# Kernel optimization log

Hardware: AMD Instinct MI355X
Metric: run time of the kernel (lower is better)

## Reference

```python
import jax, jax.numpy as jnp
import numpy as np

NUM_EMBEDDINGS = 1024
EMBEDDING_DIM = 256
SPLIT = 8
SPLIT_DIM = EMBEDDING_DIM // SPLIT  # 32
COMMITMENT_COST = 0.25
DECAY = 0.99
EPSILON = 1e-05


def setup_inputs() -> dict:
    key = jax.random.key(0)
    k1, k2, k3 = jax.random.split(key, 3)
    inputs = jax.random.normal(k1, (16384, EMBEDDING_DIM), dtype=jnp.float32)
    embedding = jax.random.normal(k2, (NUM_EMBEDDINGS, SPLIT_DIM), dtype=jnp.float32)
    ema_cluster_size = jnp.zeros((NUM_EMBEDDINGS,), dtype=jnp.float32)
    ema_w = jax.random.normal(k3, (NUM_EMBEDDINGS, SPLIT_DIM), dtype=jnp.float32)
    return {"inputs": inputs, "embedding": embedding,
            "ema_cluster_size": ema_cluster_size, "ema_w": ema_w}


def reference(inputs, embedding, ema_cluster_size, ema_w):
    B = inputs.shape[0]
    flat = inputs.reshape(-1, SPLIT_DIM)  # [B*split, d]
    rows = flat.shape[0]

    # squared euclidean distances to codebook: [rows, K]
    distances = (jnp.sum(flat ** 2, axis=1, keepdims=True)
                 + jnp.sum(embedding ** 2, axis=1)
                 - 2.0 * flat @ embedding.T)
    idx = jnp.argmin(distances, axis=1)  # [rows]

    # one-hot @ embedding == gather (same math, efficient form)
    quantized_flat = embedding[idx]  # [rows, d]

    # EMA statistics (training-mode update); quantization uses the OLD weights,
    # exactly as in the torch forward.
    counts = jax.ops.segment_sum(jnp.ones((rows,), jnp.float32), idx,
                                 num_segments=NUM_EMBEDDINGS)
    dw = jax.ops.segment_sum(flat, idx, num_segments=NUM_EMBEDDINGS)  # enc.T @ flat
    new_cs = ema_cluster_size * DECAY + (1.0 - DECAY) * counts
    n = jnp.sum(new_cs)
    new_cs = (new_cs + EPSILON) / (n + NUM_EMBEDDINGS * EPSILON) * n
    new_ema_w = ema_w * DECAY + (1.0 - DECAY) * dw
    new_embedding = new_ema_w / new_cs[:, None]

    # losses (EMA variant: only commitment term)
    e_latent_loss = jnp.mean((jax.lax.stop_gradient(quantized_flat) - flat) ** 2)
    loss = COMMITMENT_COST * e_latent_loss

    # straight-through estimator
    quantized_flat = flat + jax.lax.stop_gradient(quantized_flat - flat)
    quantized = quantized_flat.reshape(B, -1)  # [B, EMBEDDING_DIM]

    avg_probs = counts / rows  # mean of one-hot encodings over rows
    perplexity = jnp.exp(-jnp.sum(avg_probs * jnp.log(avg_probs + 1e-10)))

    encoding_indices = idx.reshape(B, SPLIT)
    return (loss, quantized, perplexity, encoding_indices,
            new_embedding, new_cs, new_ema_w)
```

## Files before the change

kernel.cpp:

```cpp
#include <hip/hip_runtime.h>

#define NUM_CODES 1024
#define DIM 32
#define ROWS 131072
#define DECAYF 0.99f
#define EPSF 1e-5f
#define CCOST 0.25f
#define SLAB 33792
#define RGROUPS 8
#define IBLK (SLAB / 256)

typedef __attribute__((ext_vector_type(8))) short short8v;
typedef __attribute__((ext_vector_type(4))) float f32x4;

__device__ __forceinline__ unsigned short bf16_rne(float f) {
    unsigned u = __float_as_uint(f);
    unsigned r = u + 0x7FFFu + ((u >> 16) & 1u);
    return (unsigned short)(r >> 16);
}

__global__ __launch_bounds__(256) void k_norms(const float* __restrict__ emb,
                                               float* __restrict__ nneg) {
    int k = blockIdx.x * 256 + threadIdx.x;
    if (k >= NUM_CODES) return;
    const float4* e4 = (const float4*)(emb + k * DIM);
    float s = 0.0f;
#pragma unroll
    for (int j = 0; j < 8; ++j) {
        float4 e = e4[j];
        s += e.x * e.x + e.y * e.y + e.z * e.z + e.w * e.w;
    }
    nneg[k] = -0.5f * s;
}

__global__ __launch_bounds__(256) void k_prep(const float* __restrict__ emb,
                                              unsigned short* __restrict__ bhi,
                                              unsigned short* __restrict__ blo) {
    int s = blockIdx.x * 256 + threadIdx.x;
    int l = s & 63, t = s >> 6;
    int code = t * 16 + (l & 15);
    int koff = (l >> 4) * 8;
    const float* src = emb + code * DIM + koff;
    float4 f0 = *(const float4*)(src);
    float4 f1 = *(const float4*)(src + 4);
    float fv[8] = {f0.x, f0.y, f0.z, f0.w, f1.x, f1.y, f1.z, f1.w};
    short8v h, lo;
#pragma unroll
    for (int j = 0; j < 8; ++j) {
        unsigned short hb = bf16_rne(fv[j]);
        float hf = __uint_as_float((unsigned)hb << 16);
        h[j]  = (short)hb;
        lo[j] = (short)bf16_rne(fv[j] - hf);
    }
    *(short8v*)(bhi + (size_t)s * 8) = h;
    *(short8v*)(blo + (size_t)s * 8) = lo;
}

__global__ __launch_bounds__(256) void k_argmin(const float* __restrict__ flat,
                                                const unsigned short* __restrict__ bhi_g,
                                                const unsigned short* __restrict__ blo_g,
                                                const float* __restrict__ nneg,
                                                int* __restrict__ idx_out,
                                                float* __restrict__ idxf_out) {
    const int lane = threadIdx.x & 63;
    const int wid  = threadIdx.x >> 6;
    const int rowbase = (blockIdx.x * 4 + wid) * 64;
    const int lr = lane & 15;
    const int lg = lane >> 4;

    short8v ahi[4], alo[4];
#pragma unroll
    for (int rf = 0; rf < 4; ++rf) {
        const float* src = flat + (size_t)(rowbase + rf * 16 + lr) * DIM + lg * 8;
        float4 f0 = *(const float4*)src;
        float4 f1 = *(const float4*)(src + 4);
        float fv[8] = {f0.x, f0.y, f0.z, f0.w, f1.x, f1.y, f1.z, f1.w};
        short8v h, lo;
#pragma unroll
        for (int j = 0; j < 8; ++j) {
            unsigned short hb = bf16_rne(fv[j]);
            float hf = __uint_as_float((unsigned)hb << 16);
            h[j]  = (short)hb;
            lo[j] = (short)bf16_rne(fv[j] - hf);
        }
        ahi[rf] = h; alo[rf] = lo;
    }

    float best[4][4];
    int   bc[4][4];
#pragma unroll
    for (int rf = 0; rf < 4; ++rf)
#pragma unroll
        for (int rg = 0; rg < 4; ++rg) { best[rf][rg] = -3.4e38f; bc[rf][rg] = 0; }

#pragma unroll 2
    for (int t = 0; t < 64; ++t) {
        short8v bh = *(const short8v*)(bhi_g + ((size_t)t * 64 + lane) * 8);
        short8v bl = *(const short8v*)(blo_g + ((size_t)t * 64 + lane) * 8);
        float nn = nneg[t * 16 + lr];
        int code = t * 16 + lr;
#pragma unroll
        for (int rf = 0; rf < 4; ++rf) {
            f32x4 acc = {nn, nn, nn, nn};
            acc = __builtin_amdgcn_mfma_f32_16x16x32_bf16(ahi[rf], bh, acc, 0, 0, 0);
            acc = __builtin_amdgcn_mfma_f32_16x16x32_bf16(ahi[rf], bl, acc, 0, 0, 0);
            acc = __builtin_amdgcn_mfma_f32_16x16x32_bf16(alo[rf], bh, acc, 0, 0, 0);
#pragma unroll
            for (int rg = 0; rg < 4; ++rg) {
                if (acc[rg] > best[rf][rg]) { best[rf][rg] = acc[rg]; bc[rf][rg] = code; }
            }
        }
    }

#pragma unroll
    for (int rf = 0; rf < 4; ++rf) {
#pragma unroll
        for (int rg = 0; rg < 4; ++rg) {
            float b = best[rf][rg];
            int   c = bc[rf][rg];
#pragma unroll
            for (int m = 1; m < 16; m <<= 1) {
                float b2 = __shfl_xor(b, m);
                int   c2 = __shfl_xor(c, m);
                if (b2 > b || (b2 == b && c2 < c)) { b = b2; c = c2; }
            }
            if (lr == rg) {
                int row = rowbase + rf * 16 + lg * 4 + rg;
                idx_out[row]  = c;
                idxf_out[row] = (float)c;
            }
        }
    }
}

__global__ __launch_bounds__(256) void k_scatter(const float* __restrict__ flat,
                                                 const float* __restrict__ emb,
                                                 const int* __restrict__ idx,
                                                 float* __restrict__ qout,
                                                 float* __restrict__ slabs,
                                                 float* __restrict__ loss_sum,
                                                 int rows_per_block) {
    __shared__ float acc[SLAB];
    __shared__ float red[256];
    const int tid = threadIdx.x;
    for (int i = tid; i < SLAB; i += 256) acc[i] = 0.0f;
    __syncthreads();

    const int row0 = blockIdx.x * rows_per_block;
    float l = 0.0f;
    for (int rr = 0; rr < rows_per_block; rr += 256) {
        int r = row0 + rr + tid;
        int k = idx[r];
        const float4* f4 = (const float4*)(flat + (size_t)r * DIM);
        const float4* e4 = (const float4*)(emb + (size_t)k * DIM);
        float4* q4 = (float4*)(qout + (size_t)r * DIM);
        int kb = k * DIM;
#pragma unroll
        for (int j4 = 0; j4 < 8; ++j4) {
            float4 f = f4[j4];
            float4 e = e4[j4];
            q4[j4] = e;
            float dx = e.x - f.x, dy = e.y - f.y, dz = e.z - f.z, dv = e.w - f.w;
            l += dx * dx + dy * dy + dz * dz + dv * dv;
            int j = 4 * j4;
            atomicAdd(&acc[kb + ((j + 0 + k) & 31)], f.x);
            atomicAdd(&acc[kb + ((j + 1 + k) & 31)], f.y);
            atomicAdd(&acc[kb + ((j + 2 + k) & 31)], f.z);
            atomicAdd(&acc[kb + ((j + 3 + k) & 31)], f.w);
        }
        atomicAdd(&acc[32768 + k], 1.0f);
    }
    __syncthreads();

    float* slab = slabs + (size_t)blockIdx.x * SLAB;
    for (int i = tid; i < 32768; i += 256) {
        int k = i >> 5, j = i & 31;
        slab[i] = acc[(i & ~31) | ((j + k) & 31)];
    }
    for (int i = tid; i < NUM_CODES; i += 256) slab[32768 + i] = acc[32768 + i];

    red[tid] = l;
    __syncthreads();
    for (int s = 128; s > 0; s >>= 1) {
        if (tid < s) red[tid] += red[tid + s];
        __syncthreads();
    }
    if (tid == 0) atomicAdd(loss_sum, red[0]);
}

__global__ __launch_bounds__(256) void k_reduce1(const float* __restrict__ slabs,
                                                 float* __restrict__ partial,
                                                 int pcount) {
    int g  = blockIdx.x / IBLK;
    int ib = blockIdx.x % IBLK;
    int i = ib * 256 + threadIdx.x;
    const float* base = slabs + (size_t)g * pcount * SLAB + i;
    float s = 0.0f;
#pragma unroll 4
    for (int p = 0; p < pcount; ++p) s += base[(size_t)p * SLAB];
    partial[(size_t)g * SLAB + i] = s;
}

__global__ __launch_bounds__(256) void k_reduce2(const float* __restrict__ partial,
                                                 float* __restrict__ dw_sum,
                                                 float* __restrict__ counts_sum) {
    int i = blockIdx.x * 256 + threadIdx.x;
    float s = 0.0f;
#pragma unroll
    for (int g = 0; g < RGROUPS; ++g) s += partial[(size_t)g * SLAB + i];
    if (i < 32768) dw_sum[i] = s;
    else           counts_sum[i - 32768] = s;
}

__global__ __launch_bounds__(1024) void k_final(const float* __restrict__ ema_cs,
                                                const float* __restrict__ ema_w,
                                                const float* __restrict__ counts,
                                                const float* __restrict__ dw,
                                                const float* __restrict__ loss_sum,
                                                float* __restrict__ out_loss,
                                                float* __restrict__ out_perp,
                                                float* __restrict__ out_emb,
                                                float* __restrict__ out_cs,
                                                float* __restrict__ out_ema_w) {
    int tid = threadIdx.x;
    __shared__ float s_cs[NUM_CODES];
    __shared__ float red[1024];

    float c = counts[tid];
    float pre = ema_cs[tid] * DECAYF + (1.0f - DECAYF) * c;

    red[tid] = pre;
    __syncthreads();
    for (int s = 512; s > 0; s >>= 1) {
        if (tid < s) red[tid] += red[tid + s];
        __syncthreads();
    }
    float n = red[0];
    __syncthreads();

    float ncs = (pre + EPSF) / (n + (float)NUM_CODES * EPSF) * n;
    s_cs[tid] = ncs;
    out_cs[tid] = ncs;

    float p = c / (float)ROWS;
    red[tid] = p * logf(p + 1e-10f);
    __syncthreads();
    for (int s = 512; s > 0; s >>= 1) {
        if (tid < s) red[tid] += red[tid + s];
        __syncthreads();
    }
    if (tid == 0) {
        out_perp[0] = expf(-red[0]);
        out_loss[0] = CCOST * (loss_sum[0] / (float)((size_t)ROWS * DIM));
    }
    __syncthreads();

    for (int i = tid; i < NUM_CODES * DIM; i += 1024) {
        int k = i >> 5;
        float w = ema_w[i] * DECAYF + (1.0f - DECAYF) * dw[i];
        out_ema_w[i] = w;
        out_emb[i] = w / s_cs[k];
    }
}

extern "C" void kernel_launch(void* const* d_in, const int* in_sizes, int n_in,
                              void* d_out, int out_size, void* d_ws, size_t ws_size,
                              hipStream_t stream) {
    const float* inputs    = (const float*)d_in[0];
    const float* embedding = (const float*)d_in[1];
    const float* ema_cs    = (const float*)d_in[2];
    const float* ema_w     = (const float*)d_in[3];

    float* out        = (float*)d_out;
    float* out_loss   = out;
    float* out_q      = out + 1;
    float* out_perp   = out + 4194305;
    float* out_idxf   = out + 4194306;
    float* out_emb    = out + 4325378;
    float* out_cs     = out + 4358146;
    float* out_ema_w  = out + 4359170;

    char* ws = (char*)d_ws;
    float* nneg       = (float*)(ws);
    float* loss_sum   = (float*)(ws + 4096);
    float* counts_sum = (float*)(ws + 8192);
    float* dw_sum     = (float*)(ws + 12288);
    int*   idx        = (int*)(ws + 143360);
    unsigned short* bhi_g = (unsigned short*)(ws + 667648);
    unsigned short* blo_g = (unsigned short*)(ws + 733184);
    float* partial    = (float*)(ws + 798720);
    float* slabs      = (float*)(ws + 1880064);

    size_t slab_off = 1880064;
    size_t avail = (ws_size > slab_off) ? (ws_size - slab_off) : 0;
    int P = 16;
    if (avail >= (size_t)256 * SLAB * 4) P = 256;
    else if (avail >= (size_t)128 * SLAB * 4) P = 128;
    else if (avail >= (size_t)64 * SLAB * 4) P = 64;
    else if (avail >= (size_t)32 * SLAB * 4) P = 32;
    int rows_per_block = ROWS / P;

    hipMemsetAsync(ws + 4096, 0, 256, stream);

    k_norms  <<<NUM_CODES / 256, 256, 0, stream>>>(embedding, nneg);
    k_prep   <<<16, 256, 0, stream>>>(embedding, bhi_g, blo_g);
    k_argmin <<<ROWS / 256, 256, 0, stream>>>(inputs, bhi_g, blo_g, nneg, idx, out_idxf);
    k_scatter<<<P, 256, 0, stream>>>(inputs, embedding, idx, out_q, slabs, loss_sum,
                                     rows_per_block);
    k_reduce1<<<RGROUPS * IBLK, 256, 0, stream>>>(slabs, partial, P / RGROUPS);
    k_reduce2<<<IBLK, 256, 0, stream>>>(partial, dw_sum, counts_sum);
    k_final  <<<1, 1024, 0, stream>>>(ema_cs, ema_w, counts_sum, dw_sum, loss_sum,
                                      out_loss, out_perp, out_emb, out_cs, out_ema_w);
}
```

Before: 109.0 us.

## Split codebook search across waves and reduce packed argmin partials in scatter

The argmin kernel now gives each block 64 rows. Its four waves each scan a quarter of the codebook tiles, which raises the wave count and shortens each wave's serial loop. Each wave writes a 64-bit key per row, made of an order-preserving distance and the code index. The scatter kernel takes the min of the four keys, which also lets it emit the float indices. The norm kernel and the memset are folded into the prep kernel to save launches. In exchange, input rows are converted redundantly in each wave, and about 8 MB of extra partial-key traffic goes through global memory.

```diff
diff --git a/kernel.cpp b/kernel.cpp
--- a/kernel.cpp
+++ b/kernel.cpp
@@ -9,6 +9,8 @@
 #define SLAB 33792
 #define RGROUPS 8
 #define IBLK (SLAB / 256)
+#define CHUNKS 4
+#define TILES_PER_CHUNK 16
 
 typedef __attribute__((ext_vector_type(8))) short short8v;
 typedef __attribute__((ext_vector_type(4))) float f32x4;
@@ -19,24 +21,23 @@
     return (unsigned short)(r >> 16);
 }
 
-__global__ __launch_bounds__(256) void k_norms(const float* __restrict__ emb,
-                                               float* __restrict__ nneg) {
-    int k = blockIdx.x * 256 + threadIdx.x;
-    if (k >= NUM_CODES) return;
-    const float4* e4 = (const float4*)(emb + k * DIM);
-    float s = 0.0f;
-#pragma unroll
-    for (int j = 0; j < 8; ++j) {
-        float4 e = e4[j];
-        s += e.x * e.x + e.y * e.y + e.z * e.z + e.w * e.w;
-    }
-    nneg[k] = -0.5f * s;
-}
-
 __global__ __launch_bounds__(256) void k_prep(const float* __restrict__ emb,
                                               unsigned short* __restrict__ bhi,
-                                              unsigned short* __restrict__ blo) {
+                                              unsigned short* __restrict__ blo,
+                                              float* __restrict__ nneg,
+                                              float* __restrict__ loss_sum) {
     int s = blockIdx.x * 256 + threadIdx.x;
+    if (s == 0) loss_sum[0] = 0.0f;
+    if (s < NUM_CODES) {
+        const float4* e4 = (const float4*)(emb + s * DIM);
+        float sum = 0.0f;
+#pragma unroll
+        for (int j = 0; j < 8; ++j) {
+            float4 e = e4[j];
+            sum += e.x * e.x + e.y * e.y + e.z * e.z + e.w * e.w;
+        }
+        nneg[s] = -0.5f * sum;
+    }
     int l = s & 63, t = s >> 6;
     int code = t * 16 + (l & 15);
     int koff = (l >> 4) * 8;
@@ -56,15 +57,14 @@
     *(short8v*)(blo + (size_t)s * 8) = lo;
 }
 
-__global__ __launch_bounds__(256) void k_argmin(const float* __restrict__ flat,
-                                                const unsigned short* __restrict__ bhi_g,
-                                                const unsigned short* __restrict__ blo_g,
-                                                const float* __restrict__ nneg,
-                                                int* __restrict__ idx_out,
-                                                float* __restrict__ idxf_out) {
+__global__ __launch_bounds__(256, 8) void k_argmin(const float* __restrict__ flat,
+                                                   const unsigned short* __restrict__ bhi_g,
+                                                   const unsigned short* __restrict__ blo_g,
+                                                   const float* __restrict__ nneg,
+                                                   unsigned long long* __restrict__ part) {
     const int lane = threadIdx.x & 63;
     const int wid  = threadIdx.x >> 6;
-    const int rowbase = (blockIdx.x * 4 + wid) * 64;
+    const int rowbase = blockIdx.x * 64;
     const int lr = lane & 15;
     const int lg = lane >> 4;
 
@@ -93,8 +93,10 @@
 #pragma unroll
         for (int rg = 0; rg < 4; ++rg) { best[rf][rg] = -3.4e38f; bc[rf][rg] = 0; }
 
+    const int t0 = wid * TILES_PER_CHUNK;
 #pragma unroll 2
-    for (int t = 0; t < 64; ++t) {
+    for (int tt = 0; tt < TILES_PER_CHUNK; ++tt) {
+        const int t = t0 + tt;
         short8v bh = *(const short8v*)(bhi_g + ((size_t)t * 64 + lane) * 8);
         short8v bl = *(const short8v*)(blo_g + ((size_t)t * 64 + lane) * 8);
         float nn = nneg[t * 16 + lr];
@@ -126,8 +128,11 @@
             }
             if (lr == rg) {
                 int row = rowbase + rf * 16 + lg * 4 + rg;
-                idx_out[row]  = c;
-                idxf_out[row] = (float)c;
+                float dist = -b;
+                unsigned du = __float_as_uint(dist);
+                du = (du & 0x80000000u) ? ~du : (du | 0x80000000u);
+                part[(size_t)wid * ROWS + row] =
+                    ((unsigned long long)du << 32) | (unsigned)c;
             }
         }
     }
@@ -135,8 +140,9 @@
 
 __global__ __launch_bounds__(256) void k_scatter(const float* __restrict__ flat,
                                                  const float* __restrict__ emb,
-                                                 const int* __restrict__ idx,
+                                                 const unsigned long long* __restrict__ part,
                                                  float* __restrict__ qout,
+                                                 float* __restrict__ idxf_out,
                                                  float* __restrict__ slabs,
                                                  float* __restrict__ loss_sum,
                                                  int rows_per_block) {
@@ -150,7 +156,14 @@
     float l = 0.0f;
     for (int rr = 0; rr < rows_per_block; rr += 256) {
         int r = row0 + rr + tid;
-        int k = idx[r];
+        unsigned long long p0 = part[r];
+        unsigned long long p1 = part[(size_t)ROWS + r];
+        unsigned long long p2 = part[2 * (size_t)ROWS + r];
+        unsigned long long p3 = part[3 * (size_t)ROWS + r];
+        unsigned long long pm = min(min(p0, p1), min(p2, p3));
+        int k = (int)(pm & 0xFFFFFFFFu);
+        idxf_out[r] = (float)k;
+
         const float4* f4 = (const float4*)(flat + (size_t)r * DIM);
         const float4* e4 = (const float4*)(emb + (size_t)k * DIM);
         float4* q4 = (float4*)(qout + (size_t)r * DIM);
@@ -285,13 +298,13 @@
     float* loss_sum   = (float*)(ws + 4096);
     float* counts_sum = (float*)(ws + 8192);
     float* dw_sum     = (float*)(ws + 12288);
-    int*   idx        = (int*)(ws + 143360);
-    unsigned short* bhi_g = (unsigned short*)(ws + 667648);
-    unsigned short* blo_g = (unsigned short*)(ws + 733184);
-    float* partial    = (float*)(ws + 798720);
-    float* slabs      = (float*)(ws + 1880064);
-
-    size_t slab_off = 1880064;
+    unsigned short* bhi_g = (unsigned short*)(ws + 143360);
+    unsigned short* blo_g = (unsigned short*)(ws + 208896);
+    unsigned long long* part = (unsigned long long*)(ws + 274432);
+    float* partial    = (float*)(ws + 4468736);
+    float* slabs      = (float*)(ws + 5550080);
+
+    size_t slab_off = 5550080;
     size_t avail = (ws_size > slab_off) ? (ws_size - slab_off) : 0;
     int P = 16;
     if (avail >= (size_t)256 * SLAB * 4) P = 256;
@@ -300,13 +313,10 @@
     else if (avail >= (size_t)32 * SLAB * 4) P = 32;
     int rows_per_block = ROWS / P;
 
-    hipMemsetAsync(ws + 4096, 0, 256, stream);
-
-    k_norms  <<<NUM_CODES / 256, 256, 0, stream>>>(embedding, nneg);
-    k_prep   <<<16, 256, 0, stream>>>(embedding, bhi_g, blo_g);
-    k_argmin <<<ROWS / 256, 256, 0, stream>>>(inputs, bhi_g, blo_g, nneg, idx, out_idxf);
-    k_scatter<<<P, 256, 0, stream>>>(inputs, embedding, idx, out_q, slabs, loss_sum,
-                                     rows_per_block);
+    k_prep   <<<16, 256, 0, stream>>>(embedding, bhi_g, blo_g, nneg, loss_sum);
+    k_argmin <<<ROWS / 64, 256, 0, stream>>>(inputs, bhi_g, blo_g, nneg, part);
+    k_scatter<<<P, 256, 0, stream>>>(inputs, embedding, part, out_q, out_idxf,
+                                     slabs, loss_sum, rows_per_block);
     k_reduce1<<<RGROUPS * IBLK, 256, 0, stream>>>(slabs, partial, P / RGROUPS);
     k_reduce2<<<IBLK, 256, 0, stream>>>(partial, dw_sum, counts_sum);
     k_final  <<<1, 1024, 0, stream>>>(ema_cs, ema_w, counts_sum, dw_sum, loss_sum,
```

Measured after the change: 402.7 us. +269.6%, slower.
